# Performance work log

Hardware: AMD Instinct MI355X
Metric: run time of the kernel (lower is better)

Reference implementation:

```python
import jax, jax.numpy as jnp
import numpy as np

EPS = 1e-6
NEG_SLOPE = 0.2
LAYER_NUM = 4
H = 128
LAT = 128


def vn_lin(x, W):
    # x: (B, C, 3, ...) ; W: (O, C) -> (B, O, 3, ...)
    return jnp.einsum('oc,bc...->bo...', W, x)


def vn_lrelu(p, d, slope):
    # VN leaky relu: project p onto half-space defined by direction d
    dot = jnp.sum(p * d, axis=2, keepdims=True)
    dsq = jnp.sum(d * d, axis=2, keepdims=True)
    p_neg = p - (dot / (dsq + EPS)) * d
    return slope * p + (1.0 - slope) * jnp.where(dot >= 0, p, p_neg)


def get_graph_feature_cross(x, k):
    # x: (B, 1, 3, N) -> (B, 3, 3, N, k)
    B, N = x.shape[0], x.shape[3]
    xf = x.reshape(B, 3, N)
    inner = -2.0 * jnp.einsum('bdi,bdj->bij', xf, xf)
    xx = jnp.sum(xf * xf, axis=1)                      # (B, N)
    neg_dist = -xx[:, :, None] - inner - xx[:, None, :]
    _, idx = jax.lax.top_k(neg_dist, k)                # (B, N, k)
    pts = jnp.transpose(xf, (0, 2, 1))                 # (B, N, 3)
    neigh = jax.vmap(lambda p, i: p[i])(pts, idx)      # (B, N, k, 3)
    center = jnp.broadcast_to(pts[:, :, None, :], neigh.shape)
    cross = jnp.cross(neigh, center)                   # torch.cross(feature, x)
    feat = jnp.stack([neigh - center, center, cross], axis=3)  # (B, N, k, 3, 3)
    return jnp.transpose(feat, (0, 3, 4, 1, 2))


def setup_inputs():
    key = jax.random.key(0)
    ks = jax.random.split(key, 11)
    B, N = 8, 1024
    def w(k, shape):
        fan_in = shape[-1]
        return jax.random.normal(k, shape, jnp.float32) / jnp.sqrt(fan_in)
    return dict(
        x=jax.random.normal(ks[0], (B, 1, N, 3), jnp.float32),
        conv_pos_Wf=w(ks[1], (H, 3)),
        conv_pos_Wd=w(ks[2], (H, 3)),
        fc_pos_W=w(ks[3], (2 * H, H)),
        blk_Wd0=w(ks[4], (LAYER_NUM, 2 * H, 2 * H)),
        blk_W0=w(ks[5], (LAYER_NUM, H, 2 * H)),
        blk_Wd1=w(ks[6], (LAYER_NUM, H, H)),
        blk_W1=w(ks[7], (LAYER_NUM, H, H)),
        blk_Ws=w(ks[8], (LAYER_NUM, H, 2 * H)),
        actvn_c_Wd=w(ks[9], (H, H)),
        fc_c_W=w(ks[10], (LAT, H)),
        num_k=20,
    )


def reference(x, conv_pos_Wf, conv_pos_Wd, fc_pos_W,
              blk_Wd0, blk_W0, blk_Wd1, blk_W1, blk_Ws,
              actvn_c_Wd, fc_c_W, num_k):
    inp = jnp.transpose(x, (0, 1, 3, 2))               # (B, 1, 3, N)
    feat = get_graph_feature_cross(inp, num_k)         # (B, 3, 3, N, k)
    # conv_pos: VNLinearLeakyReLU(3, H)
    hidden = vn_lrelu(vn_lin(feat, conv_pos_Wf), vn_lin(feat, conv_pos_Wd), NEG_SLOPE)
    hidden = jnp.mean(hidden, axis=-1)                 # pool over k -> (B, H, 3, N)
    hidden = vn_lin(hidden, fc_pos_W)                  # (B, 2H, 3, N)
    for i in range(LAYER_NUM):
        # VNResnetBlockFC(2H, H) with VN-ReLU (negative_slope=0)
        a0 = vn_lrelu(hidden, vn_lin(hidden, blk_Wd0[i]), 0.0)
        net = vn_lin(a0, blk_W0[i])                    # (B, H, 3, N)
        a1 = vn_lrelu(net, vn_lin(net, blk_Wd1[i]), 0.0)
        dx = vn_lin(a1, blk_W1[i])
        x_s = vn_lin(hidden, blk_Ws[i])                # shortcut (2H != H)
        h = x_s + dx                                   # (B, H, 3, N)
        pooled = jnp.broadcast_to(jnp.mean(h, axis=-1, keepdims=True), h.shape)
        if i < LAYER_NUM - 1:
            hidden = jnp.concatenate([h, pooled], axis=1)  # (B, 2H, 3, N)
        else:
            hidden = pooled
    hidden = jnp.mean(hidden, axis=-1)                 # (B, H, 3)
    act = vn_lrelu(hidden, vn_lin(hidden, actvn_c_Wd), NEG_SLOPE)
    return vn_lin(act, fc_c_W)                         # (B, LAT, 3)
```

## Files before the change

### kernel.cpp

```cpp
#include <hip/hip_runtime.h>
#include <cfloat>
#include <cstdint>

#define B_   8
#define N_   1024
#define H_   128
#define K_   20
#define EPS_ 1e-6f
#define R_   (B_ * 3 * N_)

typedef _Float16 half_t;
typedef _Float16 h8_t __attribute__((ext_vector_type(8)));
typedef _Float16 h4_t __attribute__((ext_vector_type(4)));
typedef __attribute__((ext_vector_type(4))) float f4_t;

__device__ inline void st4h(half_t* __restrict__ p, size_t off, f4_t v) {
    h4_t o;
    o[0] = (half_t)v[0]; o[1] = (half_t)v[1]; o[2] = (half_t)v[2]; o[3] = (half_t)v[3];
    *(h4_t*)(p + off) = o;
}

#define OFF_FC 0
#define OFF_D0 32768
#define OFF_W0 294912
#define OFF_D1 425984
#define OFF_W1 491520
#define OFF_WS 557056
#define W_TOT  688128
__global__ __launch_bounds__(256) void cvt_all(const float* __restrict__ Wfc,
                                               const float* __restrict__ Wd0,
                                               const float* __restrict__ W0,
                                               const float* __restrict__ Wd1,
                                               const float* __restrict__ W1,
                                               const float* __restrict__ Wsc,
                                               half_t* __restrict__ w) {
    int i = blockIdx.x * 256 + threadIdx.x;
    if (i >= W_TOT) return;
    const float* src; int off;
    if (i < OFF_W0)      { if (i < OFF_D0) { src = Wfc; off = OFF_FC; }
                           else            { src = Wd0; off = OFF_D0; } }
    else if (i < OFF_W1) { if (i < OFF_D1) { src = W0;  off = OFF_W0; }
                           else            { src = Wd1; off = OFF_D1; } }
    else                 { if (i < OFF_WS) { src = W1;  off = OFF_W1; }
                           else            { src = Wsc; off = OFF_WS; } }
    w[i] = (half_t)src[i - off];
}

__global__ __launch_bounds__(256) void knn_conv(const float* __restrict__ x,
                                                const float* __restrict__ Wf,
                                                const float* __restrict__ Wd,
                                                half_t* __restrict__ h1) {
    __shared__ float ps[N_ * 3];
    __shared__ int opw[4][K_];
    int t = threadIdx.x;
    int wv = t >> 6, lane = t & 63;
    int b = blockIdx.x >> 8;
    int n = (blockIdx.x & 255) * 4 + wv;

    const float4* xb4 = (const float4*)(x + (size_t)b * N_ * 3);
    float4* ps4 = (float4*)ps;
    #pragma unroll
    for (int i = 0; i < 3; ++i) ps4[t + i * 256] = xb4[t + i * 256];
    __syncthreads();

    const float cx = ps[3 * n + 0], cy = ps[3 * n + 1], cz = ps[3 * n + 2];
    uint ku[16];
    #pragma unroll
    for (int k = 0; k < 16; ++k) {
        int j = lane + (k << 6);
        const float* pj = ps + 3 * j;
        float dx = pj[0] - cx, dy = pj[1] - cy, dz = pj[2] - cz;
        float d = fmaf(dz, dz, fmaf(dy, dy, dx * dx));
        ku[k] = (__float_as_uint(d) & 0xFFFFFC00u) | (uint)j;
    }
    for (int s = 0; s < K_; ++s) {
        uint a0 = min(min(ku[0],  ku[1]),  ku[2]);
        uint a1 = min(min(ku[3],  ku[4]),  ku[5]);
        uint a2 = min(min(ku[6],  ku[7]),  ku[8]);
        uint a3 = min(min(ku[9],  ku[10]), ku[11]);
        uint a4 = min(min(ku[12], ku[13]), ku[14]);
        uint m  = min(min(min(a0, a1), min(a2, a3)), min(a4, ku[15]));
        #pragma unroll
        for (int o = 32; o; o >>= 1) m = min(m, (uint)__shfl_xor((int)m, o));
        int j = (int)(m & 1023u);
        if ((j & 63) == lane) {
            opw[wv][s] = j;
            ku[j >> 6] = 0xFFFFFFFFu;
        }
    }
    __syncthreads();

    float wf0[2], wf2[2], wd0c[2], wd2c[2];
    float bf[2][3], bg[2][3];
    #pragma unroll
    for (int c = 0; c < 2; ++c) {
        int ch = lane + c * 64;
        wf0[c]  = Wf[ch * 3 + 0];
        float wf1 = Wf[ch * 3 + 1];
        wf2[c]  = Wf[ch * 3 + 2];
        wd0c[c] = Wd[ch * 3 + 0];
        float wd1 = Wd[ch * 3 + 1];
        wd2c[c] = Wd[ch * 3 + 2];
        float df = wf1 - wf0[c], dg = wd1 - wd0c[c];
        bf[c][0] = df * cx; bf[c][1] = df * cy; bf[c][2] = df * cz;
        bg[c][0] = dg * cx; bg[c][1] = dg * cy; bg[c][2] = dg * cz;
    }
    float ax[2] = {0.f, 0.f}, ay[2] = {0.f, 0.f}, az[2] = {0.f, 0.f};
    for (int k = 0; k < K_; ++k) {
        int j = opw[wv][k];
        const float* pj = ps + 3 * j;
        float nx = pj[0], ny = pj[1], nz = pj[2];
        float rx = fmaf(ny, cz, -(nz * cy));
        float ry = fmaf(nz, cx, -(nx * cz));
        float rz = fmaf(nx, cy, -(ny * cx));
        #pragma unroll
        for (int c = 0; c < 2; ++c) {
            float fx = fmaf(wf0[c], nx, fmaf(wf2[c], rx, bf[c][0]));
            float fy = fmaf(wf0[c], ny, fmaf(wf2[c], ry, bf[c][1]));
            float fz = fmaf(wf0[c], nz, fmaf(wf2[c], rz, bf[c][2]));
            float gx = fmaf(wd0c[c], nx, fmaf(wd2c[c], rx, bg[c][0]));
            float gy = fmaf(wd0c[c], ny, fmaf(wd2c[c], ry, bg[c][1]));
            float gz = fmaf(wd0c[c], nz, fmaf(wd2c[c], rz, bg[c][2]));
            float dot = fmaf(fz, gz, fmaf(fy, gy, fx * gx));
            float dsq = fmaf(gz, gz, fmaf(gy, gy, fmaf(gx, gx, EPS_)));
            float u = fminf(dot, 0.f) * __builtin_amdgcn_rcpf(dsq) * -0.8f;
            ax[c] = fmaf(u, gx, ax[c] + fx);
            ay[c] = fmaf(u, gy, ay[c] + fy);
            az[c] = fmaf(u, gz, az[c] + fz);
        }
    }
    const float inv = 1.0f / (float)K_;
    size_t r0 = ((size_t)b * 3) * N_ + n;
    #pragma unroll
    for (int c = 0; c < 2; ++c) {
        int ch = lane + c * 64;
        h1[(r0) * H_ + ch]          = (half_t)(ax[c] * inv);
        h1[(r0 + N_) * H_ + ch]     = (half_t)(ay[c] * inv);
        h1[(r0 + 2 * N_) * H_ + ch] = (half_t)(az[c] * inv);
    }
}

__device__ inline void stsw128(half_t* __restrict__ buf, int v, int n, int o, f4_t val) {
    int phys = (((o >> 3) ^ (n & 7)) * 8) + (o & 7);
    half_t* p = buf + (v * 16 + n) * 128 + phys;
    h4_t h;
    h[0] = (half_t)val[0]; h[1] = (half_t)val[1];
    h[2] = (half_t)val[2]; h[3] = (half_t)val[3];
    *(h4_t*)p = h;
}
__device__ inline f4_t ldsw128(const half_t* __restrict__ buf, int v, int n, int o) {
    int phys = (((o >> 3) ^ (n & 7)) * 8) + (o & 7);
    const half_t* p = buf + (v * 16 + n) * 128 + phys;
    h4_t x = *(const h4_t*)p;
    f4_t r;
    r[0] = (float)x[0]; r[1] = (float)x[1]; r[2] = (float)x[2]; r[3] = (float)x[3];
    return r;
}
__device__ inline void stsw256(half_t* __restrict__ buf, int v, int n, int o, f4_t val) {
    int phys = (((o >> 3) ^ (n & 7)) * 8) + (o & 7);
    half_t* p = buf + (v * 16 + n) * 256 + phys;
    h4_t h;
    h[0] = (half_t)val[0]; h[1] = (half_t)val[1];
    h[2] = (half_t)val[2]; h[3] = (half_t)val[3];
    *(h4_t*)p = h;
}
__device__ inline f4_t ldsw256(const half_t* __restrict__ buf, int v, int n, int o) {
    int phys = (((o >> 3) ^ (n & 7)) * 8) + (o & 7);
    const half_t* p = buf + (v * 16 + n) * 256 + phys;
    h4_t x = *(const h4_t*)p;
    f4_t r;
    r[0] = (float)x[0]; r[1] = (float)x[1]; r[2] = (float)x[2]; r[3] = (float)x[3];
    return r;
}

template<bool FIRST, bool WRITE_OUT>
__global__ __launch_bounds__(512) void block_full(const half_t* __restrict__ Wfc,
                                                  const half_t* __restrict__ Wd0,
                                                  const half_t* __restrict__ W0,
                                                  const half_t* __restrict__ Wd1,
                                                  const half_t* __restrict__ Ws,
                                                  const half_t* __restrict__ W1,
                                                  const half_t* __restrict__ hprev,
                                                  const float* __restrict__ P,
                                                  const float* __restrict__ addD0,
                                                  const float* __restrict__ addWs,
                                                  half_t* __restrict__ outH,
                                                  float* __restrict__ Pp) {
    __shared__ __align__(16) char smem[FIRST ? 61440 : 49152];
    half_t* hL   = (half_t*)(smem);
    half_t* HdL  = (half_t*)(smem + 12288);
    half_t* a0L  = (half_t*)(FIRST ? smem + 36864 : smem + 12288);
    half_t* netL = (half_t*)(FIRST ? smem : smem + 36864);
    half_t* a1L  = (half_t*)(FIRST ? smem + 36864 : smem + 24576);

    const int t = threadIdx.x;
    const int lane = t & 63, wm = t >> 6;
    const int l16 = lane & 15, quad = lane >> 4;
    const int b  = blockIdx.z;
    const int nt = blockIdx.x;
    const int n0 = nt * 16;
    const size_t row0 = (size_t)(b * 3) * N_ + (n0 + l16);

    for (int c = t; c < 768; c += 512) {
        int v = c >> 8, rem = c & 255;
        int n = rem >> 4, ch = rem & 15;
        size_t g = (size_t)((b * 3 + v) * N_ + n0 + n) * 128 + ch * 8;
        *(uint4*)(hL + (v * 16 + n) * 128 + ((ch ^ (n & 7)) * 8)) =
            *(const uint4*)(hprev + g);
    }
    __syncthreads();

    if (FIRST) {
        f4_t facc[3][2];
        #pragma unroll
        for (int v = 0; v < 3; ++v)
            #pragma unroll
            for (int i = 0; i < 2; ++i)
                #pragma unroll
                for (int e = 0; e < 4; ++e) facc[v][i][e] = 0.f;
        const half_t* Af = Wfc + (size_t)(wm * 32 + l16) * 128 + quad * 8;
        #pragma unroll
        for (int k0 = 0; k0 < 128; k0 += 32) {
            h8_t ah[2], bh[3];
            #pragma unroll
            for (int i = 0; i < 2; ++i)
                ah[i] = *(const h8_t*)(Af + (size_t)i * 2048 + k0);
            int lc = (k0 >> 3) + quad;
            #pragma unroll
            for (int v = 0; v < 3; ++v)
                bh[v] = *(const h8_t*)(hL + (v * 16 + l16) * 128 + ((lc ^ (l16 & 7)) * 8));
            #pragma unroll
            for (int v = 0; v < 3; ++v)
                #pragma unroll
                for (int i = 0; i < 2; ++i)
                    facc[v][i] = __builtin_amdgcn_mfma_f32_16x16x32_f16(
                        ah[i], bh[v], facc[v][i], 0, 0, 0);
        }
        #pragma unroll
        for (int i = 0; i < 2; ++i) {
            int o = wm * 32 + i * 16 + quad * 4;
            #pragma unroll
            for (int v = 0; v < 3; ++v) stsw256(HdL, v, l16, o, facc[v][i]);
        }
        __syncthreads();
    }

    {
        constexpr int C = FIRST ? 256 : 128;
        f4_t acc[3][2];
        #pragma unroll
        for (int v = 0; v < 3; ++v)
            #pragma unroll
            for (int i = 0; i < 2; ++i)
                #pragma unroll
                for (int e = 0; e < 4; ++e) acc[v][i][e] = 0.f;

        const half_t* Ad = Wd0 + (size_t)(wm * 32 + l16) * 256 + quad * 8;
        #pragma unroll
        for (int k0 = 0; k0 < C; k0 += 32) {
            h8_t ah[2], bh[3];
            #pragma unroll
            for (int i = 0; i < 2; ++i)
                ah[i] = *(const h8_t*)(Ad + (size_t)i * 4096 + k0);
            int lc = (k0 >> 3) + quad;
            if (FIRST) {
                #pragma unroll
                for (int v = 0; v < 3; ++v)
                    bh[v] = *(const h8_t*)(HdL + (v * 16 + l16) * 256 + ((lc ^ (l16 & 7)) * 8));
            } else {
                #pragma unroll
                for (int v = 0; v < 3; ++v)
                    bh[v] = *(const h8_t*)(hL + (v * 16 + l16) * 128 + ((lc ^ (l16 & 7)) * 8));
            }
            #pragma unroll
            for (int v = 0; v < 3; ++v)
                #pragma unroll
                for (int i = 0; i < 2; ++i)
                    acc[v][i] = __builtin_amdgcn_mfma_f32_16x16x32_f16(
                        ah[i], bh[v], acc[v][i], 0, 0, 0);
        }
        #pragma unroll
        for (int i = 0; i < 2; ++i) {
            int o = wm * 32 + i * 16 + quad * 4;
            f4_t d[3], p[3];
            #pragma unroll
            for (int v = 0; v < 3; ++v) {
                d[v] = acc[v][i];
                if (!FIRST) {
                    float4 ra = *(const float4*)(addD0 + (size_t)(b * 3 + v) * 256 + o);
                    d[v][0] += ra.x; d[v][1] += ra.y; d[v][2] += ra.z; d[v][3] += ra.w;
                }
            }
            if (FIRST) {
                #pragma unroll
                for (int v = 0; v < 3; ++v)
                    p[v] = ldsw256(HdL, v, l16, o);
            } else {
                if (o < 128) {
                    #pragma unroll
                    for (int v = 0; v < 3; ++v)
                        p[v] = ldsw128(hL, v, l16, o);
                } else {
                    #pragma unroll
                    for (int e = 0; e < 4; ++e) {
                        const float* Pc = P + (size_t)(b * 128 + o - 128 + e) * 3;
                        p[0][e] = Pc[0]; p[1][e] = Pc[1]; p[2][e] = Pc[2];
                    }
                }
            }
            f4_t q[3];
            #pragma unroll
            for (int e = 0; e < 4; ++e) {
                float dot = p[0][e] * d[0][e] + p[1][e] * d[1][e] + p[2][e] * d[2][e];
                float dsq = d[0][e] * d[0][e] + d[1][e] * d[1][e] + d[2][e] * d[2][e] + EPS_;
                float cf = dot / dsq;
                if (dot >= 0.f) { q[0][e] = p[0][e]; q[1][e] = p[1][e]; q[2][e] = p[2][e]; }
                else {
                    q[0][e] = p[0][e] - cf * d[0][e];
                    q[1][e] = p[1][e] - cf * d[1][e];
                    q[2][e] = p[2][e] - cf * d[2][e];
                }
            }
            #pragma unroll
            for (int v = 0; v < 3; ++v) stsw256(a0L, v, l16, o, q[v]);
        }
    }
    __syncthreads();

    f4_t acc1[3];
    #pragma unroll
    for (int v = 0; v < 3; ++v)
        #pragma unroll
        for (int e = 0; e < 4; ++e) acc1[v][e] = 0.f;

    {
        const half_t* Aw = W0 + (size_t)(wm * 16 + l16) * 256 + quad * 8;
        #pragma unroll
        for (int k0 = 0; k0 < 256; k0 += 32) {
            h8_t ah, bh[3];
            ah = *(const h8_t*)(Aw + k0);
            int lc = (k0 >> 3) + quad;
            #pragma unroll
            for (int v = 0; v < 3; ++v)
                bh[v] = *(const h8_t*)(a0L + (v * 16 + l16) * 256 + ((lc ^ (l16 & 7)) * 8));
            #pragma unroll
            for (int v = 0; v < 3; ++v)
                acc1[v] = __builtin_amdgcn_mfma_f32_16x16x32_f16(
                    ah, bh[v], acc1[v], 0, 0, 0);
        }
    }
    {
        int o = wm * 16 + quad * 4;
        #pragma unroll
        for (int v = 0; v < 3; ++v) stsw128(netL, v, l16, o, acc1[v]);
    }
    __syncthreads();

    #pragma unroll
    for (int v = 0; v < 3; ++v)
        #pragma unroll
        for (int e = 0; e < 4; ++e) acc1[v][e] = 0.f;

    {
        const half_t* Ad1 = Wd1 + (size_t)(wm * 16 + l16) * 128 + quad * 8;
        #pragma unroll
        for (int k0 = 0; k0 < 128; k0 += 32) {
            h8_t ah, bh[3];
            ah = *(const h8_t*)(Ad1 + k0);
            int lc = (k0 >> 3) + quad;
            #pragma unroll
            for (int v = 0; v < 3; ++v)
                bh[v] = *(const h8_t*)(netL + (v * 16 + l16) * 128 + ((lc ^ (l16 & 7)) * 8));
            #pragma unroll
            for (int v = 0; v < 3; ++v)
                acc1[v] = __builtin_amdgcn_mfma_f32_16x16x32_f16(
                    ah, bh[v], acc1[v], 0, 0, 0);
        }
    }
    {
        int o = wm * 16 + quad * 4;
        f4_t p[3], q[3];
        #pragma unroll
        for (int v = 0; v < 3; ++v) p[v] = ldsw128(netL, v, l16, o);
        #pragma unroll
        for (int e = 0; e < 4; ++e) {
            float dot = p[0][e] * acc1[0][e] + p[1][e] * acc1[1][e] + p[2][e] * acc1[2][e];
            float dsq = acc1[0][e] * acc1[0][e] + acc1[1][e] * acc1[1][e]
                      + acc1[2][e] * acc1[2][e] + EPS_;
            float cf = dot / dsq;
            if (dot >= 0.f) { q[0][e] = p[0][e]; q[1][e] = p[1][e]; q[2][e] = p[2][e]; }
            else {
                q[0][e] = p[0][e] - cf * acc1[0][e];
                q[1][e] = p[1][e] - cf * acc1[1][e];
                q[2][e] = p[2][e] - cf * acc1[2][e];
            }
        }
        #pragma unroll
        for (int v = 0; v < 3; ++v) stsw128(a1L, v, l16, o, q[v]);
    }
    __syncthreads();

    #pragma unroll
    for (int v = 0; v < 3; ++v)
        #pragma unroll
        for (int e = 0; e < 4; ++e) acc1[v][e] = 0.f;

    {
        constexpr int C0 = FIRST ? 256 : 128;
        const half_t* As = Ws + (size_t)(wm * 16 + l16) * 256 + quad * 8;
        #pragma unroll
        for (int k0 = 0; k0 < C0; k0 += 32) {
            h8_t ah, bh[3];
            ah = *(const h8_t*)(As + k0);
            int lc = (k0 >> 3) + quad;
            if (FIRST) {
                #pragma unroll
                for (int v = 0; v < 3; ++v)
                    bh[v] = *(const h8_t*)(HdL + (v * 16 + l16) * 256 + ((lc ^ (l16 & 7)) * 8));
            } else {
                #pragma unroll
                for (int v = 0; v < 3; ++v)
                    bh[v] = *(const h8_t*)(hL + (v * 16 + l16) * 128 + ((lc ^ (l16 & 7)) * 8));
            }
            #pragma unroll
            for (int v = 0; v < 3; ++v)
                acc1[v] = __builtin_amdgcn_mfma_f32_16x16x32_f16(
                    ah, bh[v], acc1[v], 0, 0, 0);
        }
        const half_t* A1 = W1 + (size_t)(wm * 16 + l16) * 128 + quad * 8;
        #pragma unroll
        for (int k0 = 0; k0 < 128; k0 += 32) {
            h8_t ah, bh[3];
            ah = *(const h8_t*)(A1 + k0);
            int lc = (k0 >> 3) + quad;
            #pragma unroll
            for (int v = 0; v < 3; ++v)
                bh[v] = *(const h8_t*)(a1L + (v * 16 + l16) * 128 + ((lc ^ (l16 & 7)) * 8));
            #pragma unroll
            for (int v = 0; v < 3; ++v)
                acc1[v] = __builtin_amdgcn_mfma_f32_16x16x32_f16(
                    ah, bh[v], acc1[v], 0, 0, 0);
        }
    }

    const size_t slot = (size_t)b * 64 + nt;
    {
        int o = wm * 16 + quad * 4;
        f4_t d[3];
        #pragma unroll
        for (int v = 0; v < 3; ++v) {
            d[v] = acc1[v];
            if (!FIRST) {
                float4 ra = *(const float4*)(addWs + (size_t)(b * 3 + v) * 128 + o);
                d[v][0] += ra.x; d[v][1] += ra.y; d[v][2] += ra.z; d[v][3] += ra.w;
            }
            if (WRITE_OUT)
                st4h(outH, (row0 + (size_t)v * N_) * 128 + o, d[v]);
        }
        #pragma unroll
        for (int v = 0; v < 3; ++v)
            #pragma unroll
            for (int e = 0; e < 4; ++e) {
                float s = d[v][e];
                s += __shfl_xor(s, 1);
                s += __shfl_xor(s, 2);
                s += __shfl_xor(s, 4);
                s += __shfl_xor(s, 8);
                d[v][e] = s;
            }
        if (l16 == 0) {
            #pragma unroll
            for (int v = 0; v < 3; ++v)
                #pragma unroll
                for (int e = 0; e < 4; ++e)
                    Pp[slot * 384 + (size_t)(o + e) * 3 + v] = d[v][e];
        }
    }
}

__global__ __launch_bounds__(256) void pool_rowadd(const float* __restrict__ Pp,
                                                   const float* __restrict__ Wd0n,
                                                   const float* __restrict__ Wsn,
                                                   float* __restrict__ P,
                                                   float* __restrict__ addD0,
                                                   float* __restrict__ addWs) {
    int s = blockIdx.x;
    int b = s / 3, v = s % 3;
    int t = threadIdx.x;
    __shared__ float Pl[128];
    if (t < 128) {
        float sum = 0.f;
        const float* p = Pp + (size_t)b * 64 * 384 + (size_t)t * 3 + v;
        #pragma unroll 4
        for (int sl = 0; sl < 64; ++sl) sum += p[(size_t)sl * 384];
        sum *= (1.0f / (float)N_);
        Pl[t] = sum;
        P[(size_t)(b * 128 + t) * 3 + v] = sum;
    }
    __syncthreads();
    float sum = 0.f;
    const float* wr = Wd0n + (size_t)t * 256 + 128;
    #pragma unroll 8
    for (int c = 0; c < 128; ++c) sum += wr[c] * Pl[c];
    addD0[(size_t)s * 256 + t] = sum;
    if (t < 128) {
        const float* wr2 = Wsn + (size_t)t * 256 + 128;
        float s2 = 0.f;
        #pragma unroll 8
        for (int c = 0; c < 128; ++c) s2 += wr2[c] * Pl[c];
        addWs[(size_t)s * 128 + t] = s2;
    }
}

__global__ __launch_bounds__(128) void pool_final(const float* __restrict__ Pp,
                                                  const float* __restrict__ Wd,
                                                  const float* __restrict__ Wc,
                                                  float* __restrict__ out) {
    int b = blockIdx.x;
    int t = threadIdx.x;
    __shared__ float hid[H_][3];
    __shared__ float act[H_][3];
    {
        float s0 = 0.f, s1 = 0.f, s2 = 0.f;
        const float* p = Pp + (size_t)b * 64 * 384 + (size_t)t * 3;
        #pragma unroll 4
        for (int sl = 0; sl < 64; ++sl) {
            const float* q = p + (size_t)sl * 384;
            s0 += q[0]; s1 += q[1]; s2 += q[2];
        }
        const float inv = 1.0f / (float)N_;
        hid[t][0] = s0 * inv; hid[t][1] = s1 * inv; hid[t][2] = s2 * inv;
    }
    __syncthreads();

    float d0 = 0.f, d1 = 0.f, d2 = 0.f;
    const float* wd = Wd + (size_t)t * H_;
    for (int c = 0; c < H_; ++c) {
        float w = wd[c];
        d0 += w * hid[c][0]; d1 += w * hid[c][1]; d2 += w * hid[c][2];
    }
    float p0 = hid[t][0], p1 = hid[t][1], p2 = hid[t][2];
    float dot = p0 * d0 + p1 * d1 + p2 * d2;
    float dsq = d0 * d0 + d1 * d1 + d2 * d2 + EPS_;
    float cf = dot / dsq;
    float q0, q1, q2;
    if (dot >= 0.f) { q0 = p0; q1 = p1; q2 = p2; }
    else            { q0 = p0 - cf * d0; q1 = p1 - cf * d1; q2 = p2 - cf * d2; }
    act[t][0] = 0.2f * p0 + 0.8f * q0;
    act[t][1] = 0.2f * p1 + 0.8f * q1;
    act[t][2] = 0.2f * p2 + 0.8f * q2;
    __syncthreads();

    float o0 = 0.f, o1 = 0.f, o2 = 0.f;
    const float* wc = Wc + (size_t)t * H_;
    for (int c = 0; c < H_; ++c) {
        float w = wc[c];
        o0 += w * act[c][0]; o1 += w * act[c][1]; o2 += w * act[c][2];
    }
    size_t ob = ((size_t)b * H_ + t) * 3;
    out[ob + 0] = o0; out[ob + 1] = o1; out[ob + 2] = o2;
}

extern "C" void kernel_launch(void* const* d_in, const int* in_sizes, int n_in,
                              void* d_out, int out_size, void* d_ws, size_t ws_size,
                              hipStream_t stream) {
    const float* x   = (const float*)d_in[0];
    const float* Wf  = (const float*)d_in[1];
    const float* Wdp = (const float*)d_in[2];
    const float* Wfc = (const float*)d_in[3];
    const float* Wd0 = (const float*)d_in[4];
    const float* W0  = (const float*)d_in[5];
    const float* Wd1 = (const float*)d_in[6];
    const float* W1  = (const float*)d_in[7];
    const float* Wsc = (const float*)d_in[8];
    const float* Wda = (const float*)d_in[9];
    const float* Wc  = (const float*)d_in[10];
    float* out = (float*)d_out;
    (void)in_sizes; (void)n_in; (void)out_size; (void)ws_size;

    char* ws = (char*)d_ws;
    size_t off = 0;
    auto alloc = [&](size_t bytes) {
        void* p = ws + off;
        off = (off + bytes + 255) & ~(size_t)255;
        return p;
    };
    const size_t e128 = (size_t)R_ * 128;
    half_t* wAll  = (half_t*)alloc((size_t)W_TOT * 2);
    half_t* h1F   = (half_t*)alloc(e128 * 2);
    half_t* hF[2] = { (half_t*)alloc(e128 * 2), (half_t*)alloc(e128 * 2) };
    float*  addD0 = (float*) alloc(24 * 256 * 4);
    float*  addWs = (float*) alloc(24 * 128 * 4);
    float*  Pp    = (float*) alloc((size_t)B_ * 64 * 384 * 4);
    float*  P     = (float*) alloc((size_t)B_ * 128 * 3 * 4);

    const half_t* whFc = wAll + OFF_FC;
    const half_t* whD0 = wAll + OFF_D0;
    const half_t* whW0 = wAll + OFF_W0;
    const half_t* whD1 = wAll + OFF_D1;
    const half_t* whW1 = wAll + OFF_W1;
    const half_t* whWs = wAll + OFF_WS;

    hipLaunchKernelGGL(cvt_all, dim3((W_TOT + 255) / 256), dim3(256), 0, stream,
                       Wfc, Wd0, W0, Wd1, W1, Wsc, wAll);
    hipLaunchKernelGGL(knn_conv, dim3(B_ * N_ / 4), dim3(256), 0, stream,
                       x, Wf, Wdp, h1F);

    for (int i = 0; i < 4; ++i) {
        int cur = i & 1, prv = cur ^ 1;
        if (i == 0) {
            block_full<true, true><<<dim3(64, 1, 8), 512, 0, stream>>>(
                whFc, whD0, whW0, whD1, whWs, whW1,
                h1F, nullptr, nullptr, nullptr, hF[cur], Pp);
        } else if (i < 3) {
            block_full<false, true><<<dim3(64, 1, 8), 512, 0, stream>>>(
                whFc, whD0 + (size_t)i * 65536, whW0 + (size_t)i * 32768,
                whD1 + (size_t)i * 16384, whWs + (size_t)i * 32768,
                whW1 + (size_t)i * 16384,
                hF[prv], P, addD0, addWs, hF[cur], Pp);
        } else {
            block_full<false, false><<<dim3(64, 1, 8), 512, 0, stream>>>(
                whFc, whD0 + (size_t)i * 65536, whW0 + (size_t)i * 32768,
                whD1 + (size_t)i * 16384, whWs + (size_t)i * 32768,
                whW1 + (size_t)i * 16384,
                hF[prv], P, addD0, addWs, nullptr, Pp);
        }
        if (i < 3) {
            hipLaunchKernelGGL(pool_rowadd, dim3(24), dim3(256), 0, stream,
                               Pp, Wd0 + (size_t)(i + 1) * 65536,
                               Wsc + (size_t)(i + 1) * 32768, P, addD0, addWs);
        } else {
            hipLaunchKernelGGL(pool_final, dim3(B_), dim3(128), 0, stream,
                               Pp, Wda, Wc, out);
        }
    }
}
```

Baseline: 244.5 us.

## Fuse pooling into block kernels via last-block atomic and merge weight conversion

The separate pool_rowadd and pool_final kernels are folded into the tail of block_full. An atomic per-batch counter picks the last finishing workgroup, which then reduces the partial pools and computes the next layer's row-add terms or the final output. The fp16 weight conversion is merged into the kNN kernel as extra blocks, and those blocks also reset the counters. This removes several kernel launches and the serialization gaps between them. In exchange it adds threadfences and atomics, and the tail reduction runs on a single workgroup per batch.

```diff
diff --git a/kernel.cpp b/kernel.cpp
--- a/kernel.cpp
+++ b/kernel.cpp
@@ -27,32 +27,42 @@
 #define OFF_W1 491520
 #define OFF_WS 557056
 #define W_TOT  688128
-__global__ __launch_bounds__(256) void cvt_all(const float* __restrict__ Wfc,
-                                               const float* __restrict__ Wd0,
-                                               const float* __restrict__ W0,
-                                               const float* __restrict__ Wd1,
-                                               const float* __restrict__ W1,
-                                               const float* __restrict__ Wsc,
-                                               half_t* __restrict__ w) {
-    int i = blockIdx.x * 256 + threadIdx.x;
-    if (i >= W_TOT) return;
-    const float* src; int off;
-    if (i < OFF_W0)      { if (i < OFF_D0) { src = Wfc; off = OFF_FC; }
-                           else            { src = Wd0; off = OFF_D0; } }
-    else if (i < OFF_W1) { if (i < OFF_D1) { src = W0;  off = OFF_W0; }
-                           else            { src = Wd1; off = OFF_D1; } }
-    else                 { if (i < OFF_WS) { src = W1;  off = OFF_W1; }
-                           else            { src = Wsc; off = OFF_WS; } }
-    w[i] = (half_t)src[i - off];
-}
-
-__global__ __launch_bounds__(256) void knn_conv(const float* __restrict__ x,
-                                                const float* __restrict__ Wf,
-                                                const float* __restrict__ Wd,
-                                                half_t* __restrict__ h1) {
+#define KNN_BLKS (B_ * N_ / 4)
+#define CVT_BLKS ((W_TOT + 255) / 256)
+
+__global__ __launch_bounds__(256) void prep(const float* __restrict__ x,
+                                            const float* __restrict__ Wf,
+                                            const float* __restrict__ Wd,
+                                            half_t* __restrict__ h1,
+                                            const float* __restrict__ Wfc,
+                                            const float* __restrict__ Wd0,
+                                            const float* __restrict__ W0,
+                                            const float* __restrict__ Wd1,
+                                            const float* __restrict__ W1,
+                                            const float* __restrict__ Wsc,
+                                            half_t* __restrict__ w,
+                                            unsigned int* __restrict__ cnt) {
     __shared__ float ps[N_ * 3];
     __shared__ int opw[4][K_];
     int t = threadIdx.x;
+
+    if (blockIdx.x >= KNN_BLKS) {
+        int bid = blockIdx.x - KNN_BLKS;
+        if (bid == 0 && t < 32) cnt[t] = 0u;
+        int i = bid * 256 + t;
+        if (i < W_TOT) {
+            const float* src; int off;
+            if (i < OFF_W0)      { if (i < OFF_D0) { src = Wfc; off = OFF_FC; }
+                                   else            { src = Wd0; off = OFF_D0; } }
+            else if (i < OFF_W1) { if (i < OFF_D1) { src = W0;  off = OFF_W0; }
+                                   else            { src = Wd1; off = OFF_D1; } }
+            else                 { if (i < OFF_WS) { src = W1;  off = OFF_W1; }
+                                   else            { src = Wsc; off = OFF_WS; } }
+            w[i] = (half_t)src[i - off];
+        }
+        return;
+    }
+
     int wv = t >> 6, lane = t & 63;
     int b = blockIdx.x >> 8;
     int n = (blockIdx.x & 255) * 4 + wv;
@@ -173,7 +183,7 @@
     return r;
 }
 
-template<bool FIRST, bool WRITE_OUT>
+template<bool FIRST, bool WRITE_OUT, int POOL>
 __global__ __launch_bounds__(512) void block_full(const half_t* __restrict__ Wfc,
                                                   const half_t* __restrict__ Wd0,
                                                   const half_t* __restrict__ W0,
@@ -185,8 +195,15 @@
                                                   const float* __restrict__ addD0,
                                                   const float* __restrict__ addWs,
                                                   half_t* __restrict__ outH,
-                                                  float* __restrict__ Pp) {
+                                                  float* __restrict__ Pp,
+                                                  const float* __restrict__ PW0,
+                                                  const float* __restrict__ PW1,
+                                                  float* __restrict__ pO0,
+                                                  float* __restrict__ pO1,
+                                                  float* __restrict__ pO2,
+                                                  unsigned int* __restrict__ cnt) {
     __shared__ __align__(16) char smem[FIRST ? 61440 : 49152];
+    __shared__ unsigned int lastFlag;
     half_t* hL   = (half_t*)(smem);
     half_t* HdL  = (half_t*)(smem + 12288);
     half_t* a0L  = (half_t*)(FIRST ? smem + 36864 : smem + 12288);
@@ -476,89 +493,89 @@
                     Pp[slot * 384 + (size_t)(o + e) * 3 + v] = d[v][e];
         }
     }
-}
-
-__global__ __launch_bounds__(256) void pool_rowadd(const float* __restrict__ Pp,
-                                                   const float* __restrict__ Wd0n,
-                                                   const float* __restrict__ Wsn,
-                                                   float* __restrict__ P,
-                                                   float* __restrict__ addD0,
-                                                   float* __restrict__ addWs) {
-    int s = blockIdx.x;
-    int b = s / 3, v = s % 3;
-    int t = threadIdx.x;
-    __shared__ float Pl[128];
-    if (t < 128) {
-        float sum = 0.f;
-        const float* p = Pp + (size_t)b * 64 * 384 + (size_t)t * 3 + v;
-        #pragma unroll 4
-        for (int sl = 0; sl < 64; ++sl) sum += p[(size_t)sl * 384];
-        sum *= (1.0f / (float)N_);
-        Pl[t] = sum;
-        P[(size_t)(b * 128 + t) * 3 + v] = sum;
-    }
+
+    __threadfence();
+    if (t == 0) lastFlag = (atomicAdd(&cnt[b], 1u) == 63u) ? 1u : 0u;
     __syncthreads();
-    float sum = 0.f;
-    const float* wr = Wd0n + (size_t)t * 256 + 128;
-    #pragma unroll 8
-    for (int c = 0; c < 128; ++c) sum += wr[c] * Pl[c];
-    addD0[(size_t)s * 256 + t] = sum;
-    if (t < 128) {
-        const float* wr2 = Wsn + (size_t)t * 256 + 128;
-        float s2 = 0.f;
-        #pragma unroll 8
-        for (int c = 0; c < 128; ++c) s2 += wr2[c] * Pl[c];
-        addWs[(size_t)s * 128 + t] = s2;
-    }
-}
-
-__global__ __launch_bounds__(128) void pool_final(const float* __restrict__ Pp,
-                                                  const float* __restrict__ Wd,
-                                                  const float* __restrict__ Wc,
-                                                  float* __restrict__ out) {
-    int b = blockIdx.x;
-    int t = threadIdx.x;
-    __shared__ float hid[H_][3];
-    __shared__ float act[H_][3];
-    {
-        float s0 = 0.f, s1 = 0.f, s2 = 0.f;
-        const float* p = Pp + (size_t)b * 64 * 384 + (size_t)t * 3;
-        #pragma unroll 4
-        for (int sl = 0; sl < 64; ++sl) {
-            const float* q = p + (size_t)sl * 384;
-            s0 += q[0]; s1 += q[1]; s2 += q[2];
-        }
-        const float inv = 1.0f / (float)N_;
-        hid[t][0] = s0 * inv; hid[t][1] = s1 * inv; hid[t][2] = s2 * inv;
-    }
-    __syncthreads();
-
-    float d0 = 0.f, d1 = 0.f, d2 = 0.f;
-    const float* wd = Wd + (size_t)t * H_;
-    for (int c = 0; c < H_; ++c) {
-        float w = wd[c];
-        d0 += w * hid[c][0]; d1 += w * hid[c][1]; d2 += w * hid[c][2];
-    }
-    float p0 = hid[t][0], p1 = hid[t][1], p2 = hid[t][2];
-    float dot = p0 * d0 + p1 * d1 + p2 * d2;
-    float dsq = d0 * d0 + d1 * d1 + d2 * d2 + EPS_;
-    float cf = dot / dsq;
-    float q0, q1, q2;
-    if (dot >= 0.f) { q0 = p0; q1 = p1; q2 = p2; }
-    else            { q0 = p0 - cf * d0; q1 = p1 - cf * d1; q2 = p2 - cf * d2; }
-    act[t][0] = 0.2f * p0 + 0.8f * q0;
-    act[t][1] = 0.2f * p1 + 0.8f * q1;
-    act[t][2] = 0.2f * p2 + 0.8f * q2;
-    __syncthreads();
-
-    float o0 = 0.f, o1 = 0.f, o2 = 0.f;
-    const float* wc = Wc + (size_t)t * H_;
-    for (int c = 0; c < H_; ++c) {
-        float w = wc[c];
-        o0 += w * act[c][0]; o1 += w * act[c][1]; o2 += w * act[c][2];
-    }
-    size_t ob = ((size_t)b * H_ + t) * 3;
-    out[ob + 0] = o0; out[ob + 1] = o1; out[ob + 2] = o2;
+    if (lastFlag == 0u) return;
+    __threadfence();
+
+    if (POOL == 0) {
+        float* Pl = (float*)smem;
+        if (t < 384) {
+            int v = t >> 7, c = t & 127;
+            float sum = 0.f;
+            const float* p = Pp + (size_t)b * 64 * 384 + (size_t)c * 3 + v;
+            #pragma unroll 4
+            for (int sl = 0; sl < 64; ++sl) sum += p[(size_t)sl * 384];
+            sum *= (1.0f / (float)N_);
+            Pl[v * 128 + c] = sum;
+            pO0[(size_t)(b * 128 + c) * 3 + v] = sum;
+        }
+        __syncthreads();
+        for (int idx = t; idx < 768; idx += 512) {
+            int v = idx >> 8, t2 = idx & 255;
+            const float* wr = PW0 + (size_t)t2 * 256 + 128;
+            const float* pl = Pl + v * 128;
+            float sum = 0.f;
+            #pragma unroll 8
+            for (int c = 0; c < 128; ++c) sum += wr[c] * pl[c];
+            pO1[(size_t)(b * 3 + v) * 256 + t2] = sum;
+        }
+        if (t < 384) {
+            int v = t >> 7, t2 = t & 127;
+            const float* wr2 = PW1 + (size_t)t2 * 256 + 128;
+            const float* pl = Pl + v * 128;
+            float s2 = 0.f;
+            #pragma unroll 8
+            for (int c = 0; c < 128; ++c) s2 += wr2[c] * pl[c];
+            pO2[(size_t)(b * 3 + v) * 128 + t2] = s2;
+        }
+    } else {
+        float* hid = (float*)smem;
+        float* act = hid + 384;
+        if (t < 128) {
+            float s0 = 0.f, s1 = 0.f, s2 = 0.f;
+            const float* p = Pp + (size_t)b * 64 * 384 + (size_t)t * 3;
+            #pragma unroll 4
+            for (int sl = 0; sl < 64; ++sl) {
+                const float* q = p + (size_t)sl * 384;
+                s0 += q[0]; s1 += q[1]; s2 += q[2];
+            }
+            const float inv = 1.0f / (float)N_;
+            hid[t * 3 + 0] = s0 * inv; hid[t * 3 + 1] = s1 * inv; hid[t * 3 + 2] = s2 * inv;
+        }
+        __syncthreads();
+        if (t < 128) {
+            float d0 = 0.f, d1 = 0.f, d2 = 0.f;
+            const float* wd = PW0 + (size_t)t * H_;
+            for (int c = 0; c < H_; ++c) {
+                float w = wd[c];
+                d0 += w * hid[c * 3 + 0]; d1 += w * hid[c * 3 + 1]; d2 += w * hid[c * 3 + 2];
+            }
+            float p0 = hid[t * 3 + 0], p1 = hid[t * 3 + 1], p2 = hid[t * 3 + 2];
+            float dot = p0 * d0 + p1 * d1 + p2 * d2;
+            float dsq = d0 * d0 + d1 * d1 + d2 * d2 + EPS_;
+            float cf = dot / dsq;
+            float q0, q1, q2;
+            if (dot >= 0.f) { q0 = p0; q1 = p1; q2 = p2; }
+            else            { q0 = p0 - cf * d0; q1 = p1 - cf * d1; q2 = p2 - cf * d2; }
+            act[t * 3 + 0] = 0.2f * p0 + 0.8f * q0;
+            act[t * 3 + 1] = 0.2f * p1 + 0.8f * q1;
+            act[t * 3 + 2] = 0.2f * p2 + 0.8f * q2;
+        }
+        __syncthreads();
+        if (t < 128) {
+            float o0 = 0.f, o1 = 0.f, o2 = 0.f;
+            const float* wc = PW1 + (size_t)t * H_;
+            for (int c = 0; c < H_; ++c) {
+                float w = wc[c];
+                o0 += w * act[c * 3 + 0]; o1 += w * act[c * 3 + 1]; o2 += w * act[c * 3 + 2];
+            }
+            size_t ob = ((size_t)b * H_ + t) * 3;
+            pO0[ob + 0] = o0; pO0[ob + 1] = o1; pO0[ob + 2] = o2;
+        }
+    }
 }
 
 extern "C" void kernel_launch(void* const* d_in, const int* in_sizes, int n_in,
@@ -593,6 +610,7 @@
     float*  addWs = (float*) alloc(24 * 128 * 4);
     float*  Pp    = (float*) alloc((size_t)B_ * 64 * 384 * 4);
     float*  P     = (float*) alloc((size_t)B_ * 128 * 3 * 4);
+    unsigned int* cnt = (unsigned int*)alloc(32 * 4);
 
     const half_t* whFc = wAll + OFF_FC;
     const half_t* whD0 = wAll + OFF_D0;
@@ -601,37 +619,32 @@
     const half_t* whW1 = wAll + OFF_W1;
     const half_t* whWs = wAll + OFF_WS;
 
-    hipLaunchKernelGGL(cvt_all, dim3((W_TOT + 255) / 256), dim3(256), 0, stream,
-                       Wfc, Wd0, W0, Wd1, W1, Wsc, wAll);
-    hipLaunchKernelGGL(knn_conv, dim3(B_ * N_ / 4), dim3(256), 0, stream,
-                       x, Wf, Wdp, h1F);
+    hipLaunchKernelGGL(prep, dim3(KNN_BLKS + CVT_BLKS), dim3(256), 0, stream,
+                       x, Wf, Wdp, h1F, Wfc, Wd0, W0, Wd1, W1, Wsc, wAll, cnt);
 
     for (int i = 0; i < 4; ++i) {
         int cur = i & 1, prv = cur ^ 1;
         if (i == 0) {
-            block_full<true, true><<<dim3(64, 1, 8), 512, 0, stream>>>(
+            block_full<true, true, 0><<<dim3(64, 1, 8), 512, 0, stream>>>(
                 whFc, whD0, whW0, whD1, whWs, whW1,
-                h1F, nullptr, nullptr, nullptr, hF[cur], Pp);
+                h1F, nullptr, nullptr, nullptr, hF[cur], Pp,
+                Wd0 + (size_t)1 * 65536, Wsc + (size_t)1 * 32768,
+                P, addD0, addWs, cnt + 0);
         } else if (i < 3) {
-            block_full<false, true><<<dim3(64, 1, 8), 512, 0, stream>>>(
+            block_full<false, true, 0><<<dim3(64, 1, 8), 512, 0, stream>>>(
                 whFc, whD0 + (size_t)i * 65536, whW0 + (size_t)i * 32768,
                 whD1 + (size_t)i * 16384, whWs + (size_t)i * 32768,
                 whW1 + (size_t)i * 16384,
-                hF[prv], P, addD0, addWs, hF[cur], Pp);
+                hF[prv], P, addD0, addWs, hF[cur], Pp,
+                Wd0 + (size_t)(i + 1) * 65536, Wsc + (size_t)(i + 1) * 32768,
+                P, addD0, addWs, cnt + i * 8);
         } else {
-            block_full<false, false><<<dim3(64, 1, 8), 512, 0, stream>>>(
+            block_full<false, false, 1><<<dim3(64, 1, 8), 512, 0, stream>>>(
                 whFc, whD0 + (size_t)i * 65536, whW0 + (size_t)i * 32768,
                 whD1 + (size_t)i * 16384, whWs + (size_t)i * 32768,
                 whW1 + (size_t)i * 16384,
-                hF[prv], P, addD0, addWs, nullptr, Pp);
-        }
-        if (i < 3) {
-            hipLaunchKernelGGL(pool_rowadd, dim3(24), dim3(256), 0, stream,
-                               Pp, Wd0 + (size_t)(i + 1) * 65536,
-                               Wsc + (size_t)(i + 1) * 32768, P, addD0, addWs);
-        } else {
-            hipLaunchKernelGGL(pool_final, dim3(B_), dim3(128), 0, stream,
-                               Pp, Wda, Wc, out);
-        }
-    }
-}
+                hF[prv], P, addD0, addWs, nullptr, Pp,
+                Wda, Wc, out, nullptr, nullptr, cnt + 24);
+        }
+    }
+}
```

Result: slower. 739.8 us (+202.5%).

## Fuse pooling/rowadd into block kernels and merge weight conversion into kNN launch

Applied to the files above, without the earlier changes.

Removes the separate pool_rowadd kernels by having each non-first block kernel recompute the pooled means and the pooled-channel matvecs (Wd0, Ws halves) into shared memory at its start. It also merges the fp32-to-fp16 weight conversion into the kNN kernel launch as extra blocks. This cuts kernel launches and inter-kernel gaps. The cost is that every one of the 512 blocks redundantly repeats the pooling reduction and 128x384 matvecs from fp32 global memory, and an extra barrier is added. Pooled partials now go to a separate buffer per layer to avoid overwriting.

```diff
diff --git a/kernel.cpp b/kernel.cpp
--- a/kernel.cpp
+++ b/kernel.cpp
@@ -27,32 +27,40 @@
 #define OFF_W1 491520
 #define OFF_WS 557056
 #define W_TOT  688128
-__global__ __launch_bounds__(256) void cvt_all(const float* __restrict__ Wfc,
-                                               const float* __restrict__ Wd0,
-                                               const float* __restrict__ W0,
-                                               const float* __restrict__ Wd1,
-                                               const float* __restrict__ W1,
-                                               const float* __restrict__ Wsc,
-                                               half_t* __restrict__ w) {
-    int i = blockIdx.x * 256 + threadIdx.x;
-    if (i >= W_TOT) return;
-    const float* src; int off;
-    if (i < OFF_W0)      { if (i < OFF_D0) { src = Wfc; off = OFF_FC; }
-                           else            { src = Wd0; off = OFF_D0; } }
-    else if (i < OFF_W1) { if (i < OFF_D1) { src = W0;  off = OFF_W0; }
-                           else            { src = Wd1; off = OFF_D1; } }
-    else                 { if (i < OFF_WS) { src = W1;  off = OFF_W1; }
-                           else            { src = Wsc; off = OFF_WS; } }
-    w[i] = (half_t)src[i - off];
-}
-
-__global__ __launch_bounds__(256) void knn_conv(const float* __restrict__ x,
-                                                const float* __restrict__ Wf,
-                                                const float* __restrict__ Wd,
-                                                half_t* __restrict__ h1) {
+#define KNN_BLKS (B_ * N_ / 4)
+#define CVT_BLKS ((W_TOT + 255) / 256)
+
+__global__ __launch_bounds__(256) void prep(const float* __restrict__ x,
+                                            const float* __restrict__ Wf,
+                                            const float* __restrict__ Wd,
+                                            half_t* __restrict__ h1,
+                                            const float* __restrict__ Wfc,
+                                            const float* __restrict__ Wd0,
+                                            const float* __restrict__ W0,
+                                            const float* __restrict__ Wd1,
+                                            const float* __restrict__ W1,
+                                            const float* __restrict__ Wsc,
+                                            half_t* __restrict__ w) {
     __shared__ float ps[N_ * 3];
     __shared__ int opw[4][K_];
     int t = threadIdx.x;
+
+    if (blockIdx.x >= KNN_BLKS) {
+        int bid = blockIdx.x - KNN_BLKS;
+        int i = bid * 256 + t;
+        if (i < W_TOT) {
+            const float* src; int off;
+            if (i < OFF_W0)      { if (i < OFF_D0) { src = Wfc; off = OFF_FC; }
+                                   else            { src = Wd0; off = OFF_D0; } }
+            else if (i < OFF_W1) { if (i < OFF_D1) { src = W0;  off = OFF_W0; }
+                                   else            { src = Wd1; off = OFF_D1; } }
+            else                 { if (i < OFF_WS) { src = W1;  off = OFF_W1; }
+                                   else            { src = Wsc; off = OFF_WS; } }
+            w[i] = (half_t)src[i - off];
+        }
+        return;
+    }
+
     int wv = t >> 6, lane = t & 63;
     int b = blockIdx.x >> 8;
     int n = (blockIdx.x & 255) * 4 + wv;
@@ -181,17 +189,20 @@
                                                   const half_t* __restrict__ Ws,
                                                   const half_t* __restrict__ W1,
                                                   const half_t* __restrict__ hprev,
-                                                  const float* __restrict__ P,
-                                                  const float* __restrict__ addD0,
-                                                  const float* __restrict__ addWs,
+                                                  const float* __restrict__ PpPrev,
+                                                  const float* __restrict__ PW0,
+                                                  const float* __restrict__ PW1,
                                                   half_t* __restrict__ outH,
-                                                  float* __restrict__ Pp) {
-    __shared__ __align__(16) char smem[FIRST ? 61440 : 49152];
+                                                  float* __restrict__ PpOut) {
+    __shared__ __align__(16) char smem[FIRST ? 61440 : 50688];
     half_t* hL   = (half_t*)(smem);
     half_t* HdL  = (half_t*)(smem + 12288);
     half_t* a0L  = (half_t*)(FIRST ? smem + 36864 : smem + 12288);
     half_t* netL = (half_t*)(FIRST ? smem : smem + 36864);
     half_t* a1L  = (half_t*)(FIRST ? smem + 36864 : smem + 24576);
+    float* plP  = (float*)(smem + 12288);
+    float* plD0 = (float*)(smem + 12288 + 1536);
+    float* plWs = (float*)(smem + 49152);
 
     const int t = threadIdx.x;
     const int lane = t & 63, wm = t >> 6;
@@ -208,6 +219,37 @@
         *(uint4*)(hL + (v * 16 + n) * 128 + ((ch ^ (n & 7)) * 8)) =
             *(const uint4*)(hprev + g);
     }
+
+    if (!FIRST) {
+        if (t < 384) {
+            int v = t >> 7, c = t & 127;
+            float sum = 0.f;
+            const float* p = PpPrev + (size_t)b * 64 * 384 + (size_t)c * 3 + v;
+            #pragma unroll 4
+            for (int sl = 0; sl < 64; ++sl) sum += p[(size_t)sl * 384];
+            sum *= (1.0f / (float)N_);
+            plP[v * 128 + c] = sum;
+        }
+        __syncthreads();
+        for (int idx = t; idx < 768; idx += 512) {
+            int v = idx >> 8, t2 = idx & 255;
+            const float* wr = PW0 + (size_t)t2 * 256 + 128;
+            const float* pl = plP + v * 128;
+            float sum = 0.f;
+            #pragma unroll 8
+            for (int c = 0; c < 128; ++c) sum += wr[c] * pl[c];
+            plD0[v * 256 + t2] = sum;
+        }
+        if (t < 384) {
+            int v = t >> 7, t2 = t & 127;
+            const float* wr2 = PW1 + (size_t)t2 * 256 + 128;
+            const float* pl = plP + v * 128;
+            float s2 = 0.f;
+            #pragma unroll 8
+            for (int c = 0; c < 128; ++c) s2 += wr2[c] * pl[c];
+            plWs[v * 128 + t2] = s2;
+        }
+    }
     __syncthreads();
 
     if (FIRST) {
@@ -279,6 +321,7 @@
                     acc[v][i] = __builtin_amdgcn_mfma_f32_16x16x32_f16(
                         ah[i], bh[v], acc[v][i], 0, 0, 0);
         }
+        f4_t qs[2][3];
         #pragma unroll
         for (int i = 0; i < 2; ++i) {
             int o = wm * 32 + i * 16 + quad * 4;
@@ -287,8 +330,8 @@
             for (int v = 0; v < 3; ++v) {
                 d[v] = acc[v][i];
                 if (!FIRST) {
-                    float4 ra = *(const float4*)(addD0 + (size_t)(b * 3 + v) * 256 + o);
-                    d[v][0] += ra.x; d[v][1] += ra.y; d[v][2] += ra.z; d[v][3] += ra.w;
+                    #pragma unroll
+                    for (int e = 0; e < 4; ++e) d[v][e] += plD0[v * 256 + o + e];
                 }
             }
             if (FIRST) {
@@ -303,26 +346,32 @@
                 } else {
                     #pragma unroll
                     for (int e = 0; e < 4; ++e) {
-                        const float* Pc = P + (size_t)(b * 128 + o - 128 + e) * 3;
-                        p[0][e] = Pc[0]; p[1][e] = Pc[1]; p[2][e] = Pc[2];
+                        p[0][e] = plP[0 * 128 + o - 128 + e];
+                        p[1][e] = plP[1 * 128 + o - 128 + e];
+                        p[2][e] = plP[2 * 128 + o - 128 + e];
                     }
                 }
             }
-            f4_t q[3];
             #pragma unroll
             for (int e = 0; e < 4; ++e) {
                 float dot = p[0][e] * d[0][e] + p[1][e] * d[1][e] + p[2][e] * d[2][e];
                 float dsq = d[0][e] * d[0][e] + d[1][e] * d[1][e] + d[2][e] * d[2][e] + EPS_;
                 float cf = dot / dsq;
-                if (dot >= 0.f) { q[0][e] = p[0][e]; q[1][e] = p[1][e]; q[2][e] = p[2][e]; }
-                else {
-                    q[0][e] = p[0][e] - cf * d[0][e];
-                    q[1][e] = p[1][e] - cf * d[1][e];
-                    q[2][e] = p[2][e] - cf * d[2][e];
+                if (dot >= 0.f) {
+                    qs[i][0][e] = p[0][e]; qs[i][1][e] = p[1][e]; qs[i][2][e] = p[2][e];
+                } else {
+                    qs[i][0][e] = p[0][e] - cf * d[0][e];
+                    qs[i][1][e] = p[1][e] - cf * d[1][e];
+                    qs[i][2][e] = p[2][e] - cf * d[2][e];
                 }
             }
-            #pragma unroll
-            for (int v = 0; v < 3; ++v) stsw256(a0L, v, l16, o, q[v]);
+        }
+        if (!FIRST) __syncthreads();
+        #pragma unroll
+        for (int i = 0; i < 2; ++i) {
+            int o = wm * 32 + i * 16 + quad * 4;
+            #pragma unroll
+            for (int v = 0; v < 3; ++v) stsw256(a0L, v, l16, o, qs[i][v]);
         }
     }
     __syncthreads();
@@ -345,8 +394,7 @@
                 bh[v] = *(const h8_t*)(a0L + (v * 16 + l16) * 256 + ((lc ^ (l16 & 7)) * 8));
             #pragma unroll
             for (int v = 0; v < 3; ++v)
-                acc1[v] = __builtin_amdgcn_mfma_f32_16x16x32_f16(
-                    ah, bh[v], acc1[v], 0, 0, 0);
+                acc1[v] = __builtin_amdgcn_mfma_f32_16x16x32_f16(ah, bh[v], acc1[v], 0, 0, 0);
         }
     }
     {
@@ -373,8 +421,7 @@
                 bh[v] = *(const h8_t*)(netL + (v * 16 + l16) * 128 + ((lc ^ (l16 & 7)) * 8));
             #pragma unroll
             for (int v = 0; v < 3; ++v)
-                acc1[v] = __builtin_amdgcn_mfma_f32_16x16x32_f16(
-                    ah, bh[v], acc1[v], 0, 0, 0);
+                acc1[v] = __builtin_amdgcn_mfma_f32_16x16x32_f16(ah, bh[v], acc1[v], 0, 0, 0);
         }
     }
     {
@@ -424,8 +471,7 @@
             }
             #pragma unroll
             for (int v = 0; v < 3; ++v)
-                acc1[v] = __builtin_amdgcn_mfma_f32_16x16x32_f16(
-                    ah, bh[v], acc1[v], 0, 0, 0);
+                acc1[v] = __builtin_amdgcn_mfma_f32_16x16x32_f16(ah, bh[v], acc1[v], 0, 0, 0);
         }
         const half_t* A1 = W1 + (size_t)(wm * 16 + l16) * 128 + quad * 8;
         #pragma unroll
@@ -438,8 +484,7 @@
                 bh[v] = *(const h8_t*)(a1L + (v * 16 + l16) * 128 + ((lc ^ (l16 & 7)) * 8));
             #pragma unroll
             for (int v = 0; v < 3; ++v)
-                acc1[v] = __builtin_amdgcn_mfma_f32_16x16x32_f16(
-                    ah, bh[v], acc1[v], 0, 0, 0);
+                acc1[v] = __builtin_amdgcn_mfma_f32_16x16x32_f16(ah, bh[v], acc1[v], 0, 0, 0);
         }
     }
 
@@ -451,8 +496,8 @@
         for (int v = 0; v < 3; ++v) {
             d[v] = acc1[v];
             if (!FIRST) {
-                float4 ra = *(const float4*)(addWs + (size_t)(b * 3 + v) * 128 + o);
-                d[v][0] += ra.x; d[v][1] += ra.y; d[v][2] += ra.z; d[v][3] += ra.w;
+                #pragma unroll
+                for (int e = 0; e < 4; ++e) d[v][e] += plWs[v * 128 + o + e];
             }
             if (WRITE_OUT)
                 st4h(outH, (row0 + (size_t)v * N_) * 128 + o, d[v]);
@@ -473,42 +518,8 @@
             for (int v = 0; v < 3; ++v)
                 #pragma unroll
                 for (int e = 0; e < 4; ++e)
-                    Pp[slot * 384 + (size_t)(o + e) * 3 + v] = d[v][e];
-        }
-    }
-}
-
-__global__ __launch_bounds__(256) void pool_rowadd(const float* __restrict__ Pp,
-                                                   const float* __restrict__ Wd0n,
-                                                   const float* __restrict__ Wsn,
-                                                   float* __restrict__ P,
-                                                   float* __restrict__ addD0,
-                                                   float* __restrict__ addWs) {
-    int s = blockIdx.x;
-    int b = s / 3, v = s % 3;
-    int t = threadIdx.x;
-    __shared__ float Pl[128];
-    if (t < 128) {
-        float sum = 0.f;
-        const float* p = Pp + (size_t)b * 64 * 384 + (size_t)t * 3 + v;
-        #pragma unroll 4
-        for (int sl = 0; sl < 64; ++sl) sum += p[(size_t)sl * 384];
-        sum *= (1.0f / (float)N_);
-        Pl[t] = sum;
-        P[(size_t)(b * 128 + t) * 3 + v] = sum;
-    }
-    __syncthreads();
-    float sum = 0.f;
-    const float* wr = Wd0n + (size_t)t * 256 + 128;
-    #pragma unroll 8
-    for (int c = 0; c < 128; ++c) sum += wr[c] * Pl[c];
-    addD0[(size_t)s * 256 + t] = sum;
-    if (t < 128) {
-        const float* wr2 = Wsn + (size_t)t * 256 + 128;
-        float s2 = 0.f;
-        #pragma unroll 8
-        for (int c = 0; c < 128; ++c) s2 += wr2[c] * Pl[c];
-        addWs[(size_t)s * 128 + t] = s2;
+                    PpOut[slot * 384 + (size_t)(o + e) * 3 + v] = d[v][e];
+        }
     }
 }
 
@@ -586,13 +597,11 @@
         return p;
     };
     const size_t e128 = (size_t)R_ * 128;
+    const size_t ppSl = (size_t)B_ * 64 * 384;
     half_t* wAll  = (half_t*)alloc((size_t)W_TOT * 2);
     half_t* h1F   = (half_t*)alloc(e128 * 2);
     half_t* hF[2] = { (half_t*)alloc(e128 * 2), (half_t*)alloc(e128 * 2) };
-    float*  addD0 = (float*) alloc(24 * 256 * 4);
-    float*  addWs = (float*) alloc(24 * 128 * 4);
-    float*  Pp    = (float*) alloc((size_t)B_ * 64 * 384 * 4);
-    float*  P     = (float*) alloc((size_t)B_ * 128 * 3 * 4);
+    float*  Pp    = (float*) alloc(4 * ppSl * 4);
 
     const half_t* whFc = wAll + OFF_FC;
     const half_t* whD0 = wAll + OFF_D0;
@@ -601,10 +610,8 @@
     const half_t* whW1 = wAll + OFF_W1;
     const half_t* whWs = wAll + OFF_WS;
 
-    hipLaunchKernelGGL(cvt_all, dim3((W_TOT + 255) / 256), dim3(256), 0, stream,
-                       Wfc, Wd0, W0, Wd1, W1, Wsc, wAll);
-    hipLaunchKernelGGL(knn_conv, dim3(B_ * N_ / 4), dim3(256), 0, stream,
-                       x, Wf, Wdp, h1F);
+    hipLaunchKernelGGL(prep, dim3(KNN_BLKS + CVT_BLKS), dim3(256), 0, stream,
+                       x, Wf, Wdp, h1F, Wfc, Wd0, W0, Wd1, W1, Wsc, wAll);
 
     for (int i = 0; i < 4; ++i) {
         int cur = i & 1, prv = cur ^ 1;
@@ -617,21 +624,19 @@
                 whFc, whD0 + (size_t)i * 65536, whW0 + (size_t)i * 32768,
                 whD1 + (size_t)i * 16384, whWs + (size_t)i * 32768,
                 whW1 + (size_t)i * 16384,
-                hF[prv], P, addD0, addWs, hF[cur], Pp);
+                hF[prv], Pp + (size_t)(i - 1) * ppSl,
+                Wd0 + (size_t)i * 65536, Wsc + (size_t)i * 32768,
+                hF[cur], Pp + (size_t)i * ppSl);
         } else {
             block_full<false, false><<<dim3(64, 1, 8), 512, 0, stream>>>(
                 whFc, whD0 + (size_t)i * 65536, whW0 + (size_t)i * 32768,
                 whD1 + (size_t)i * 16384, whWs + (size_t)i * 32768,
                 whW1 + (size_t)i * 16384,
-                hF[prv], P, addD0, addWs, nullptr, Pp);
-        }
-        if (i < 3) {
-            hipLaunchKernelGGL(pool_rowadd, dim3(24), dim3(256), 0, stream,
-                               Pp, Wd0 + (size_t)(i + 1) * 65536,
-                               Wsc + (size_t)(i + 1) * 32768, P, addD0, addWs);
-        } else {
-            hipLaunchKernelGGL(pool_final, dim3(B_), dim3(128), 0, stream,
-                               Pp, Wda, Wc, out);
-        }
-    }
-}
+                hF[prv], Pp + (size_t)(i - 1) * ppSl,
+                Wd0 + (size_t)i * 65536, Wsc + (size_t)i * 32768,
+                nullptr, Pp + (size_t)i * ppSl);
+        }
+    }
+    hipLaunchKernelGGL(pool_final, dim3(B_), dim3(128), 0, stream,
+                       Pp + (size_t)3 * ppSl, Wda, Wc, out);
+}
```

New measurement: 306.7 us. +25.4%, slower.
